# Performance work log

Hardware: AMD Instinct MI355X
Metric: run time of the kernel (lower is better)

Reference implementation:

```python
import jax, jax.numpy as jnp
import numpy as np

N0, N1, N2 = 100000, 25000, 5000
E0, E1 = 400000, 80000
IN_FEATS, N_HIDDEN, N_CLASSES = 512, 512, 64


def setup_inputs() -> dict:
    key = jax.random.key(0)
    ks = jax.random.split(key, 16)
    return {
        "feats": jax.random.normal(ks[0], (N0, IN_FEATS), jnp.float32),
        "h0_hist": jax.random.normal(ks[1], (N0, N_HIDDEN), jnp.float32),
        "agg_h0": jax.random.normal(ks[2], (N1, N_HIDDEN), jnp.float32),
        "h1_hist": jax.random.normal(ks[3], (N1, 2 * N_HIDDEN), jnp.float32),
        "agg_h1": jax.random.normal(ks[4], (N2, 2 * N_HIDDEN), jnp.float32),
        "W0": jax.random.normal(ks[5], (N_HIDDEN, IN_FEATS), jnp.float32) * 0.02,
        "b0": jax.random.normal(ks[6], (N_HIDDEN,), jnp.float32) * 0.02,
        "W1": jax.random.normal(ks[7], (N_HIDDEN, N_HIDDEN), jnp.float32) * 0.02,
        "b1": jax.random.normal(ks[8], (N_HIDDEN,), jnp.float32) * 0.02,
        "W2": jax.random.normal(ks[9], (N_CLASSES, 2 * N_HIDDEN), jnp.float32) * 0.02,
        "b2": jax.random.normal(ks[10], (N_CLASSES,), jnp.float32) * 0.02,
        "src0": jax.random.randint(ks[11], (E0,), 0, N0, jnp.int64),
        "dst0": jax.random.randint(ks[12], (E0,), 0, N1, jnp.int64),
        "src1": jax.random.randint(ks[13], (E1,), 0, N1, jnp.int64),
        "dst1": jax.random.randint(ks[14], (E1,), 0, N2, jnp.int64),
    }


def _segment_mean(h_src, src, dst, num_dst):
    # copy_src gather + variable-degree mean reduction (DGL fn.mean)
    msg = h_src[src]  # [E, D]
    sums = jax.ops.segment_sum(msg, dst, num_segments=num_dst)
    deg = jax.ops.segment_sum(jnp.ones((src.shape[0],), h_src.dtype), dst,
                              num_segments=num_dst)
    return sums / jnp.maximum(deg, 1.0)[:, None]


def reference(feats, h0_hist, agg_h0, h1_hist, agg_h1,
              W0, b0, W1, b1, W2, b2,
              src0, dst0, src1, dst1):
    # input layer: linear + relu (dropout=0)
    h = jax.nn.relu(feats @ W0.T + b0)  # [N0, H]

    # block 0: control-variate subtract, mean-aggregate, NodeUpdate(1) concat
    h = h - h0_hist
    agg = _segment_mean(h, src0, dst0, agg_h0.shape[0])  # [N1, H]
    h = (agg + agg_h0) @ W1.T + b1
    h = jnp.concatenate([h, jax.nn.relu(h)], axis=1)  # [N1, 2H]

    # block 1: control-variate subtract, mean-aggregate, NodeUpdate(2)
    h = h - h1_hist
    agg = _segment_mean(h, src1, dst1, agg_h1.shape[0])  # [N2, 2H]
    h = (agg + agg_h1) @ W2.T + b2  # [N2, C]
    return h
```

## Files before the change

### kernel.cpp

```cpp
#include <hip/hip_runtime.h>

#define N0c 100000
#define N1c 25000
#define N2c 5000
#define E0c 400000
#define E1c 80000

typedef __attribute__((ext_vector_type(8))) short bf16x8;
typedef __attribute__((ext_vector_type(4))) float f32x4;

#define GLOAD_LDS(g, l) \
    __builtin_amdgcn_global_load_lds((__attribute__((address_space(1))) const unsigned int*)(const void*)(g), \
                                     (__attribute__((address_space(3))) unsigned int*)(void*)(l), 16, 0, 0)

static __device__ __forceinline__ uint rnd_bf(float f) {
    uint u = __float_as_uint(f);
    return (u + 0x7FFFu + ((u >> 16) & 1u)) & 0xFFFF0000u;
}
static __device__ __forceinline__ unsigned short to_bf(float f) {
    return (unsigned short)(rnd_bf(f) >> 16);
}
static __device__ __forceinline__ uint cvt2bf(float f0, float f1) {
    uint r;
    asm("v_cvt_pk_bf16_f32 %0, %1, %2" : "=v"(r) : "v"(f0), "v"(f1));
    return r;
}

__global__ __launch_bounds__(256)
void presplit_w(const float* __restrict__ X, uint4* __restrict__ out)
{
    const int id = blockIdx.x * 256 + threadIdx.x;
    const int nh = id >> 14;
    const int rem = id & 16383;
    const int kt = rem >> 10;
    const int sl = rem & 1023;
    const int R = sl >> 2, p = sl & 3;
    const int o = p ^ ((R >> 1) & 3);
    const float* src = X + (size_t)(nh * 256 + R) * 512 + kt * 32 + o * 8;
    float4 x0 = *(const float4*)src;
    float4 x1 = *(const float4*)(src + 4);
    uint4 v;
    v.x = cvt2bf(x0.x, x0.y); v.y = cvt2bf(x0.z, x0.w);
    v.z = cvt2bf(x1.x, x1.y); v.w = cvt2bf(x1.z, x1.w);
    out[id] = v;
}

template<int ASRC, int EPI>
__global__ __launch_bounds__(512)
void gemm_fused(const float* __restrict__ Af32, const uint4* __restrict__ At,
                const uint4* __restrict__ Bt, const float* __restrict__ bias,
                const float* __restrict__ hist, unsigned short* __restrict__ C,
                int Mreal, int nblk)
{
    constexpr int ABASE = (ASRC == 0) ? 1024 : 512;
    __shared__ uint4 lds[(ASRC == 0) ? 2048 : 1536];

    const int tid = threadIdx.x;
    const int orig = blockIdx.x;
    const int xcd = orig & 7, q = nblk >> 3, rr = nblk & 7;
    const int lid = (xcd < rr ? xcd * (q + 1) : rr * (q + 1) + (xcd - rr) * q) + (orig >> 3);
    const int bm = lid >> 1, bnh = lid & 1;

    const int w = tid >> 6, lane = tid & 63;
    const int wm = w >> 2, wn = w & 3;
    const int lg = lane >> 4, lr = lane & 15;

    f32x4 acc[4][4];
#pragma unroll
    for (int i = 0; i < 4; ++i)
#pragma unroll
        for (int j = 0; j < 4; ++j) acc[i][j] = {0.f, 0.f, 0.f, 0.f};

    for (int kt = 0; kt < 16; ++kt) {
        if (kt) __syncthreads();
        if (ASRC == 0) {
#pragma unroll
            for (int j = 0; j < 2; ++j) {
                const int slot = w * 128 + j * 64 + lane;
                const int r = slot >> 3, p = slot & 7;
                const int t = p ^ (r & 7);
                const int o = ((t & 3) << 1) | (t >> 2);
                int g = bm * 128 + r; if (g > Mreal - 1) g = Mreal - 1;
                GLOAD_LDS(Af32 + (size_t)g * 512 + kt * 32 + o * 4, &lds[slot]);
            }
        } else {
            if (tid < 512)
                GLOAD_LDS(At + ((size_t)bm * 16 + kt) * 512 + tid, &lds[tid]);
        }
        {
            const uint4* Bsrc = Bt + ((size_t)bnh * 16 + kt) * 1024;
#pragma unroll
            for (int j = 0; j < 2; ++j) {
                const int slot = w * 128 + j * 64 + lane;
                GLOAD_LDS(Bsrc + slot, &lds[ABASE + slot]);
            }
        }
        __syncthreads();

        bf16x8 a[4], b[4];
#pragma unroll
        for (int mi = 0; mi < 4; ++mi) {
            const int r = wm * 64 + mi * 16 + lr;
            if (ASRC == 0) {
                const int sw = r & 7;
                const uint4* rp = &lds[r * 8];
                const f32x4 q0 = *(const f32x4*)&rp[lg ^ sw];
                const f32x4 q1 = *(const f32x4*)&rp[(lg + 4) ^ sw];
                uint4 v;
                v.x = cvt2bf(q0[0], q0[1]); v.y = cvt2bf(q0[2], q0[3]);
                v.z = cvt2bf(q1[0], q1[1]); v.w = cvt2bf(q1[2], q1[3]);
                a[mi] = *(const bf16x8*)&v;
            } else {
                a[mi] = *(const bf16x8*)&lds[r * 4 + (lg ^ ((r >> 1) & 3))];
            }
        }
#pragma unroll
        for (int ni = 0; ni < 4; ++ni) {
            const int R = wn * 64 + ni * 16 + lr;
            b[ni] = *(const bf16x8*)&lds[ABASE + R * 4 + (lg ^ ((R >> 1) & 3))];
        }
#pragma unroll
        for (int mi = 0; mi < 4; ++mi)
#pragma unroll
            for (int ni = 0; ni < 4; ++ni)
                acc[mi][ni] = __builtin_amdgcn_mfma_f32_16x16x32_bf16(
                    a[mi], b[ni], acc[mi][ni], 0, 0, 0);
    }

#pragma unroll
    for (int mi = 0; mi < 4; ++mi)
#pragma unroll
        for (int ni = 0; ni < 4; ++ni) {
            const int col = bnh * 256 + wn * 64 + ni * 16 + lr;
            const float bv = bias[col];
#pragma unroll
            for (int r = 0; r < 4; ++r) {
                const int m = bm * 128 + wm * 64 + mi * 16 + lg * 4 + r;
                if (m < Mreal) {
                    const float v = acc[mi][ni][r] + bv;
                    if (EPI == 0) {
                        C[(size_t)m * 512 + col] = to_bf(fmaxf(v, 0.f) - hist[(size_t)m * 512 + col]);
                    } else {
                        C[(size_t)m * 1024 + col]       = to_bf(v - hist[(size_t)m * 1024 + col]);
                        C[(size_t)m * 1024 + 512 + col] = to_bf(fmaxf(v, 0.f) - hist[(size_t)m * 1024 + 512 + col]);
                    }
                }
            }
        }
}

__global__ __launch_bounds__(256)
void gemm64(const float* __restrict__ A, const float* __restrict__ B,
            const float* __restrict__ bias, float* __restrict__ C, int M)
{
    const int K = 1024;
    __shared__ float As[32][68];
    __shared__ float Bs[32][68];
    const int tid = threadIdx.x;
    const int tx = tid & 15, ty = tid >> 4;
    const int lrow = tid >> 3;
    const int lk   = (tid & 7) * 4;
    const int bm = blockIdx.x;

    float acc[4][4];
#pragma unroll
    for (int i = 0; i < 4; ++i)
#pragma unroll
        for (int j = 0; j < 4; ++j) acc[i][j] = 0.f;

    int ar0 = bm * 64 + lrow;      if (ar0 > M - 1) ar0 = M - 1;
    int ar1 = bm * 64 + 32 + lrow; if (ar1 > M - 1) ar1 = M - 1;

    for (int kt = 0; kt < K; kt += 32) {
        float4 a0 = *(const float4*)(A + (size_t)ar0 * K + kt + lk);
        float4 a1 = *(const float4*)(A + (size_t)ar1 * K + kt + lk);
        float4 b0 = *(const float4*)(B + (size_t)lrow * K + kt + lk);
        float4 b1 = *(const float4*)(B + (size_t)(32 + lrow) * K + kt + lk);
        __syncthreads();
        As[lk+0][lrow]    = a0.x; As[lk+1][lrow]    = a0.y; As[lk+2][lrow]    = a0.z; As[lk+3][lrow]    = a0.w;
        As[lk+0][lrow+32] = a1.x; As[lk+1][lrow+32] = a1.y; As[lk+2][lrow+32] = a1.z; As[lk+3][lrow+32] = a1.w;
        Bs[lk+0][lrow]    = b0.x; Bs[lk+1][lrow]    = b0.y; Bs[lk+2][lrow]    = b0.z; Bs[lk+3][lrow]    = b0.w;
        Bs[lk+0][lrow+32] = b1.x; Bs[lk+1][lrow+32] = b1.y; Bs[lk+2][lrow+32] = b1.z; Bs[lk+3][lrow+32] = b1.w;
        __syncthreads();
#pragma unroll
        for (int kk = 0; kk < 32; ++kk) {
            float4 av = *(const float4*)&As[kk][ty * 4];
            float4 bv = *(const float4*)&Bs[kk][tx * 4];
            float aa[4] = {av.x, av.y, av.z, av.w};
            float bb[4] = {bv.x, bv.y, bv.z, bv.w};
#pragma unroll
            for (int i = 0; i < 4; ++i)
#pragma unroll
                for (int j = 0; j < 4; ++j)
                    acc[i][j] += aa[i] * bb[j];
        }
    }

    const float4 bv = *(const float4*)&bias[tx * 4];
#pragma unroll
    for (int i = 0; i < 4; ++i) {
        const int m = bm * 64 + ty * 4 + i;
        if (m >= M) continue;
        float4 o;
        o.x = acc[i][0] + bv.x; o.y = acc[i][1] + bv.y;
        o.z = acc[i][2] + bv.z; o.w = acc[i][3] + bv.w;
        *(float4*)&C[(size_t)m * 64 + tx * 4] = o;
    }
}

__global__ void count_deg(const int* __restrict__ dst, int* __restrict__ deg, int E)
{
    int e = blockIdx.x * blockDim.x + threadIdx.x;
    if (e < E) atomicAdd(&deg[dst[e]], 1);
}

__global__ __launch_bounds__(1024)
void exscan(const int* __restrict__ deg, int* __restrict__ off, int* __restrict__ cur, int n)
{
    __shared__ int wsum[16];
    __shared__ int carry;
    const int tid = threadIdx.x, lane = tid & 63, w = tid >> 6;
    if (tid == 0) carry = 0;
    __syncthreads();
    for (int base = 0; base < n; base += 1024) {
        const int i = base + tid;
        const int v = (i < n) ? deg[i] : 0;
        int x = v;
#pragma unroll
        for (int d = 1; d < 64; d <<= 1) {
            int y = __shfl_up(x, d, 64);
            if (lane >= d) x += y;
        }
        if (lane == 63) wsum[w] = x;
        __syncthreads();
        int wo = 0, tot = 0;
#pragma unroll
        for (int k = 0; k < 16; ++k) { int s = wsum[k]; tot += s; if (k < w) wo += s; }
        const int excl = carry + wo + x - v;
        if (i < n) { off[i] = excl; cur[i] = excl; }
        __syncthreads();
        if (tid == 0) carry += tot;
        __syncthreads();
    }
    if (tid == 0) off[n] = carry;
}

__global__ void scatter_edges(const int* __restrict__ src, const int* __restrict__ dst,
                              int* __restrict__ cur, int* __restrict__ eidx, int E)
{
    int e = blockIdx.x * blockDim.x + threadIdx.x;
    if (e < E) {
        int p = atomicAdd(&cur[dst[e]], 1);
        eidx[p] = src[e];
    }
}

__global__ __launch_bounds__(256)
void seg_mean_split(const unsigned short* __restrict__ h, const int* __restrict__ off,
                    const int* __restrict__ eidx, const float* __restrict__ addin,
                    uint4* __restrict__ out, int n_dst, int n_pad)
{
    const int wid = blockIdx.x * 4 + (threadIdx.x >> 6);
    const int lane = threadIdx.x & 63;
    if (wid >= n_pad) return;
    uint4 v = {0u, 0u, 0u, 0u};
    if (wid < n_dst) {
        const int e0 = off[wid], e1 = off[wid + 1];
        float s[8];
#pragma unroll
        for (int i = 0; i < 8; ++i) s[i] = 0.f;
        for (int e = e0; e < e1; ++e) {
            const uint4 vv = *((const uint4*)(h + (size_t)eidx[e] * 512) + lane);
            const uint u[4] = {vv.x, vv.y, vv.z, vv.w};
#pragma unroll
            for (int i = 0; i < 4; ++i) {
                s[2 * i]     += __uint_as_float(u[i] << 16);
                s[2 * i + 1] += __uint_as_float(u[i] & 0xFFFF0000u);
            }
        }
        const float sc = 1.0f / (float)((e1 - e0) > 0 ? (e1 - e0) : 1);
        const float* ad = addin + (size_t)wid * 512 + lane * 8;
        float4 d0 = *(const float4*)ad;
        float4 d1 = *(const float4*)(ad + 4);
        v.x = cvt2bf(s[0] * sc + d0.x, s[1] * sc + d0.y);
        v.y = cvt2bf(s[2] * sc + d0.z, s[3] * sc + d0.w);
        v.z = cvt2bf(s[4] * sc + d1.x, s[5] * sc + d1.y);
        v.w = cvt2bf(s[6] * sc + d1.z, s[7] * sc + d1.w);
    }
    const int mt = wid >> 7, r = wid & 127;
    const int kt = lane >> 2, o = lane & 3;
    out[((size_t)mt * 16 + kt) * 512 + r * 4 + (o ^ ((r >> 1) & 3))] = v;
}

__global__ __launch_bounds__(256)
void seg_mean_add4(const unsigned short* __restrict__ h, const int* __restrict__ off,
                   const int* __restrict__ eidx, const float* __restrict__ addin,
                   float* __restrict__ out, int n_dst)
{
    const int wid = blockIdx.x * 4 + (threadIdx.x >> 6);
    const int lane = threadIdx.x & 63;
    if (wid >= n_dst) return;
    const int e0 = off[wid], e1 = off[wid + 1];
    float s[16];
#pragma unroll
    for (int i = 0; i < 16; ++i) s[i] = 0.f;
    for (int e = e0; e < e1; ++e) {
        const uint4* row = (const uint4*)(h + (size_t)eidx[e] * 1024);
#pragma unroll
        for (int half = 0; half < 2; ++half) {
            const uint4 v = row[lane + 64 * half];
            const uint u[4] = {v.x, v.y, v.z, v.w};
#pragma unroll
            for (int i = 0; i < 4; ++i) {
                s[8 * half + 2 * i]     += __uint_as_float(u[i] << 16);
                s[8 * half + 2 * i + 1] += __uint_as_float(u[i] & 0xFFFF0000u);
            }
        }
    }
    const float sc = 1.0f / (float)((e1 - e0) > 0 ? (e1 - e0) : 1);
#pragma unroll
    for (int half = 0; half < 2; ++half) {
        const float* ad = addin + (size_t)wid * 1024 + half * 512 + lane * 8;
        float* o = out + (size_t)wid * 1024 + half * 512 + lane * 8;
        float4 d0 = *(const float4*)ad;
        float4 d1 = *(const float4*)(ad + 4);
        float4 r0, r1;
        r0.x = s[8*half+0] * sc + d0.x; r0.y = s[8*half+1] * sc + d0.y;
        r0.z = s[8*half+2] * sc + d0.z; r0.w = s[8*half+3] * sc + d0.w;
        r1.x = s[8*half+4] * sc + d1.x; r1.y = s[8*half+5] * sc + d1.y;
        r1.z = s[8*half+6] * sc + d1.z; r1.w = s[8*half+7] * sc + d1.w;
        *(float4*)o = r0;
        *(float4*)(o + 4) = r1;
    }
}

extern "C" void kernel_launch(void* const* d_in, const int* in_sizes, int n_in,
                              void* d_out, int out_size, void* d_ws, size_t ws_size,
                              hipStream_t stream)
{
    const float* feats   = (const float*)d_in[0];
    const float* h0_hist = (const float*)d_in[1];
    const float* agg_h0  = (const float*)d_in[2];
    const float* h1_hist = (const float*)d_in[3];
    const float* agg_h1  = (const float*)d_in[4];
    const float* W0 = (const float*)d_in[5];
    const float* b0 = (const float*)d_in[6];
    const float* W1 = (const float*)d_in[7];
    const float* b1 = (const float*)d_in[8];
    const float* W2 = (const float*)d_in[9];
    const float* b2 = (const float*)d_in[10];
    const int* src0 = (const int*)d_in[11];
    const int* dst0 = (const int*)d_in[12];
    const int* src1 = (const int*)d_in[13];
    const int* dst1 = (const int*)d_in[14];

    const int MT1 = 782;
    const int MT2 = 196;

    const size_t h0B   = ((size_t)N0c * 512 * 2 + 255) & ~(size_t)255;
    const size_t a2B   = (size_t)MT2 * 16 * 512 * 16;
    const size_t agg1B = (size_t)N2c * 1024 * 4;
    const size_t wsB   = 32768 * 16;

    char* ws = (char*)d_ws;
    unsigned short* h0 = (unsigned short*)ws;
    unsigned short* h1cat = h0;                              ws += h0B;
    uint4* A2s    = (uint4*)ws;                              ws += a2B;
    float* agg1   = (float*)ws;                              ws += agg1B;
    uint4* Ws0    = (uint4*)ws;                              ws += wsB;
    uint4* Ws1    = (uint4*)ws;                              ws += wsB;
    int* deg0  = (int*)ws;  ws += sizeof(int) * N1c;
    int* off0  = (int*)ws;  ws += sizeof(int) * (N1c + 1);
    int* cur0  = (int*)ws;  ws += sizeof(int) * N1c;
    int* eidx0 = (int*)ws;  ws += sizeof(int) * E0c;
    int* deg1  = (int*)ws;  ws += sizeof(int) * N2c;
    int* off1  = (int*)ws;  ws += sizeof(int) * (N2c + 1);
    int* cur1  = (int*)ws;  ws += sizeof(int) * N2c;
    int* eidx1 = (int*)ws;

    hipMemsetAsync(deg0, 0, sizeof(int) * N1c, stream);
    hipMemsetAsync(deg1, 0, sizeof(int) * N2c, stream);

    presplit_w<<<128, 256, 0, stream>>>(W0, Ws0);
    presplit_w<<<128, 256, 0, stream>>>(W1, Ws1);
    count_deg<<<(E0c + 255) / 256, 256, 0, stream>>>(dst0, deg0, E0c);
    exscan<<<1, 1024, 0, stream>>>(deg0, off0, cur0, N1c);
    scatter_edges<<<(E0c + 255) / 256, 256, 0, stream>>>(src0, dst0, cur0, eidx0, E0c);

    gemm_fused<0, 0><<<MT1 * 2, 512, 0, stream>>>(feats, nullptr, Ws0, b0, h0_hist, h0, N0c, MT1 * 2);

    seg_mean_split<<<(MT2 * 128) / 4, 256, 0, stream>>>(h0, off0, eidx0, agg_h0, A2s, N1c, MT2 * 128);

    count_deg<<<(E1c + 255) / 256, 256, 0, stream>>>(dst1, deg1, E1c);
    exscan<<<1, 1024, 0, stream>>>(deg1, off1, cur1, N2c);
    scatter_edges<<<(E1c + 255) / 256, 256, 0, stream>>>(src1, dst1, cur1, eidx1, E1c);

    gemm_fused<1, 1><<<MT2 * 2, 512, 0, stream>>>(nullptr, A2s, Ws1, b1, h1_hist, h1cat, N1c, MT2 * 2);

    seg_mean_add4<<<(N2c + 3) / 4, 256, 0, stream>>>(h1cat, off1, eidx1, agg_h1, agg1, N2c);

    gemm64<<<(N2c + 63) / 64, 256, 0, stream>>>(agg1, W2, b2, (float*)d_out, N2c);
}
```

Measured before the change: 576.6 us.

## Double-buffer LDS tiles in fused GEMM to overlap loads with MFMA

The GEMM main loop now uses two LDS buffers. The next k-tile's global-to-LDS loads are issued before the MFMAs on the current tile, with a single vmcnt wait and barrier at the end of each iteration. This hides global load latency behind compute and removes one of the two barriers per iteration. In exchange it doubles LDS use per block, which may lower occupancy, particularly for the fp32 A-source variant.

```diff
diff --git a/kernel.cpp b/kernel.cpp
--- a/kernel.cpp
+++ b/kernel.cpp
@@ -53,7 +53,8 @@
                 int Mreal, int nblk)
 {
     constexpr int ABASE = (ASRC == 0) ? 1024 : 512;
-    __shared__ uint4 lds[(ASRC == 0) ? 2048 : 1536];
+    constexpr int BUF   = ABASE + 1024;
+    __shared__ uint4 lds[2 * BUF];
 
     const int tid = threadIdx.x;
     const int orig = blockIdx.x;
@@ -65,37 +66,46 @@
     const int wm = w >> 2, wn = w & 3;
     const int lg = lane >> 4, lr = lane & 15;
 
+    const int s_slot = w * 128 + lane;
+    const int s_r0 = s_slot >> 3, s_p0 = s_slot & 7;
+    const int s_r1 = (s_slot + 64) >> 3, s_p1 = (s_slot + 64) & 7;
+
+    auto stage = [&](int kt, int base) {
+        if (ASRC == 0) {
+            {
+                const int t = s_p0 ^ (s_r0 & 7);
+                const int o = ((t & 3) << 1) | (t >> 2);
+                int g = bm * 128 + s_r0; if (g > Mreal - 1) g = Mreal - 1;
+                GLOAD_LDS(Af32 + (size_t)g * 512 + kt * 32 + o * 4, &lds[base + s_slot]);
+            }
+            {
+                const int t = s_p1 ^ (s_r1 & 7);
+                const int o = ((t & 3) << 1) | (t >> 2);
+                int g = bm * 128 + s_r1; if (g > Mreal - 1) g = Mreal - 1;
+                GLOAD_LDS(Af32 + (size_t)g * 512 + kt * 32 + o * 4, &lds[base + s_slot + 64]);
+            }
+        } else {
+            GLOAD_LDS(At + ((size_t)bm * 16 + kt) * 512 + tid, &lds[base + tid]);
+        }
+        const uint4* Bsrc = Bt + ((size_t)bnh * 16 + kt) * 1024;
+        GLOAD_LDS(Bsrc + s_slot, &lds[base + ABASE + s_slot]);
+        GLOAD_LDS(Bsrc + s_slot + 64, &lds[base + ABASE + s_slot + 64]);
+    };
+
     f32x4 acc[4][4];
 #pragma unroll
     for (int i = 0; i < 4; ++i)
 #pragma unroll
         for (int j = 0; j < 4; ++j) acc[i][j] = {0.f, 0.f, 0.f, 0.f};
 
+    stage(0, 0);
+    asm volatile("s_waitcnt vmcnt(0)" ::: "memory");
+    __builtin_amdgcn_s_barrier();
+    asm volatile("" ::: "memory");
+
     for (int kt = 0; kt < 16; ++kt) {
-        if (kt) __syncthreads();
-        if (ASRC == 0) {
-#pragma unroll
-            for (int j = 0; j < 2; ++j) {
-                const int slot = w * 128 + j * 64 + lane;
-                const int r = slot >> 3, p = slot & 7;
-                const int t = p ^ (r & 7);
-                const int o = ((t & 3) << 1) | (t >> 2);
-                int g = bm * 128 + r; if (g > Mreal - 1) g = Mreal - 1;
-                GLOAD_LDS(Af32 + (size_t)g * 512 + kt * 32 + o * 4, &lds[slot]);
-            }
-        } else {
-            if (tid < 512)
-                GLOAD_LDS(At + ((size_t)bm * 16 + kt) * 512 + tid, &lds[tid]);
-        }
-        {
-            const uint4* Bsrc = Bt + ((size_t)bnh * 16 + kt) * 1024;
-#pragma unroll
-            for (int j = 0; j < 2; ++j) {
-                const int slot = w * 128 + j * 64 + lane;
-                GLOAD_LDS(Bsrc + slot, &lds[ABASE + slot]);
-            }
-        }
-        __syncthreads();
+        const int cb = (kt & 1) * BUF;
+        if (kt < 15) stage(kt + 1, ((kt + 1) & 1) * BUF);
 
         bf16x8 a[4], b[4];
 #pragma unroll
@@ -103,7 +113,7 @@
             const int r = wm * 64 + mi * 16 + lr;
             if (ASRC == 0) {
                 const int sw = r & 7;
-                const uint4* rp = &lds[r * 8];
+                const uint4* rp = &lds[cb + r * 8];
                 const f32x4 q0 = *(const f32x4*)&rp[lg ^ sw];
                 const f32x4 q1 = *(const f32x4*)&rp[(lg + 4) ^ sw];
                 uint4 v;
@@ -111,13 +121,13 @@
                 v.z = cvt2bf(q1[0], q1[1]); v.w = cvt2bf(q1[2], q1[3]);
                 a[mi] = *(const bf16x8*)&v;
             } else {
-                a[mi] = *(const bf16x8*)&lds[r * 4 + (lg ^ ((r >> 1) & 3))];
+                a[mi] = *(const bf16x8*)&lds[cb + r * 4 + (lg ^ ((r >> 1) & 3))];
             }
         }
 #pragma unroll
         for (int ni = 0; ni < 4; ++ni) {
             const int R = wn * 64 + ni * 16 + lr;
-            b[ni] = *(const bf16x8*)&lds[ABASE + R * 4 + (lg ^ ((R >> 1) & 3))];
+            b[ni] = *(const bf16x8*)&lds[cb + ABASE + R * 4 + (lg ^ ((R >> 1) & 3))];
         }
 #pragma unroll
         for (int mi = 0; mi < 4; ++mi)
@@ -125,6 +135,12 @@
             for (int ni = 0; ni < 4; ++ni)
                 acc[mi][ni] = __builtin_amdgcn_mfma_f32_16x16x32_bf16(
                     a[mi], b[ni], acc[mi][ni], 0, 0, 0);
+
+        if (kt < 15) {
+            asm volatile("s_waitcnt vmcnt(0)" ::: "memory");
+            __builtin_amdgcn_s_barrier();
+            asm volatile("" ::: "memory");
+        }
     }
 
 #pragma unroll
```

Measured after the change: 566.5 us. No clear change (-1.7%).
